# Performance work log

Measured on AMD Instinct MI355X. Metric: run time of the kernel, lower is better.

## Reference

```python
import jax, jax.numpy as jnp
import numpy as np

B, NV, L, NKG = 8, 100, 128, 923
NT = NV + 1 + NKG  # 1024 total nodes
DV, DK, DH, H, NLAYERS, VOCAB = 2048, 300, 1024, 8, 3, 50265
DHD = DH // H


def _ln(x, g, b, eps=1e-5):
    m = x.mean(-1, keepdims=True)
    v = x.var(-1, keepdims=True)
    return (x - m) / jnp.sqrt(v + eps) * g + b


def _gat_layer(x, mask, W, bb, a_src, a_dst, ln_g, ln_b):
    # x: [B,N,D], mask: [B,N,N] bool
    Bn, N, D = x.shape
    h = (x @ W + bb).reshape(Bn, N, H, DHD)
    s = jnp.einsum('bnhd,hd->bnh', h, a_src)  # source term
    t = jnp.einsum('bnhd,hd->bnh', h, a_dst)  # target term
    e = jax.nn.leaky_relu(s[:, :, None, :] + t[:, None, :, :], 0.2)  # [B,N,N,H]
    e = jnp.where(mask[..., None], e, -1e9)
    a = jax.nn.softmax(e, axis=2)  # over neighbors j
    out = jnp.einsum('bijh,bjhd->bihd', a, h).reshape(Bn, N, D)
    return _ln(x + out, ln_g, ln_b)


def setup_inputs() -> dict:
    key = jax.random.key(0)
    ks = jax.random.split(key, 24)
    s = 0.02
    inp = {
        'visual_features': jax.random.normal(ks[0], (B, NV, DV), jnp.float32),
        'question_input_ids': jax.random.randint(ks[1], (B, L), 0, VOCAB, jnp.int64) if False else jax.random.randint(ks[1], (B, L), 0, VOCAB).astype(jnp.int32),
        'question_attention_mask': jnp.ones((B, L), jnp.int32),
        'graph_node_features': jax.random.normal(ks[2], (B, NKG, DK), jnp.float32),
        'graph_adj': jax.random.randint(ks[3], (B, NT, NT), 0, 2).astype(jnp.int32),
        'graph_node_types': jax.random.randint(ks[4], (B, NT), 0, 3).astype(jnp.int32),
        # params
        'vis_W': jax.random.normal(ks[5], (DV, DH), jnp.float32) * s,
        'vis_b': jnp.zeros((DH,), jnp.float32),
        'vis_ln_g': jnp.ones((DH,), jnp.float32),
        'vis_ln_b': jnp.zeros((DH,), jnp.float32),
        'tok_emb': jax.random.normal(ks[6], (VOCAB, DH), jnp.float32) * s,
        'q_W': jax.random.normal(ks[7], (DH, DH), jnp.float32) * s,
        'q_b': jnp.zeros((DH,), jnp.float32),
        'q_ln_g': jnp.ones((DH,), jnp.float32),
        'q_ln_b': jnp.zeros((DH,), jnp.float32),
        'kg_W': jax.random.normal(ks[8], (DK, DH), jnp.float32) * s,
        'kg_b': jnp.zeros((DH,), jnp.float32),
        'kg_ln_g': jnp.ones((DH,), jnp.float32),
        'kg_ln_b': jnp.zeros((DH,), jnp.float32),
        'type_emb': jax.random.normal(ks[9], (3, DH), jnp.float32) * s,
        'gat_W': jax.random.normal(ks[10], (NLAYERS, DH, DH), jnp.float32) * s,
        'gat_b': jnp.zeros((NLAYERS, DH), jnp.float32),
        'a_src': jax.random.normal(ks[11], (NLAYERS, H, DHD), jnp.float32) * s,
        'a_dst': jax.random.normal(ks[12], (NLAYERS, H, DHD), jnp.float32) * s,
        'gat_ln_g': jnp.ones((NLAYERS, DH), jnp.float32),
        'gat_ln_b': jnp.zeros((NLAYERS, DH), jnp.float32),
        'readout_W': jax.random.normal(ks[13], (DH, 1), jnp.float32) * s,
        'readout_b': jnp.zeros((1,), jnp.float32),
        'cs_W1': jax.random.normal(ks[14], (DH, DH), jnp.float32) * s,
        'cs_b1': jnp.zeros((DH,), jnp.float32),
        'cs_W2': jax.random.normal(ks[15], (DH, 1), jnp.float32) * s,
        'cs_b2': jnp.zeros((1,), jnp.float32),
    }
    return inp


def reference(visual_features, question_input_ids, question_attention_mask,
              graph_node_features, graph_adj, graph_node_types,
              vis_W, vis_b, vis_ln_g, vis_ln_b,
              tok_emb, q_W, q_b, q_ln_g, q_ln_b,
              kg_W, kg_b, kg_ln_g, kg_ln_b,
              type_emb, gat_W, gat_b, a_src, a_dst, gat_ln_g, gat_ln_b,
              readout_W, readout_b, cs_W1, cs_b1, cs_W2, cs_b2):
    # 1. visual projection
    vis = _ln(visual_features @ vis_W + vis_b, vis_ln_g, vis_ln_b)  # [B,NV,DH]
    # 2. text encoder (embedding + masked mean-pool + proj + LN)
    te = tok_emb[question_input_ids]  # [B,L,DH]
    m = question_attention_mask.astype(te.dtype)[..., None]
    pooled = (te * m).sum(1) / jnp.maximum(m.sum(1), 1.0)
    q = _ln(pooled @ q_W + q_b, q_ln_g, q_ln_b)[:, None, :]  # [B,1,DH]
    # 3. KG projection
    kg = _ln(graph_node_features @ kg_W + kg_b, kg_ln_g, kg_ln_b)
    # 4-5. concat + node-type embeddings
    x = jnp.concatenate([vis, q, kg], axis=1) + type_emb[graph_node_types]
    # 6. dense GAT stack
    mask = graph_adj > 0
    for l in range(NLAYERS):
        x = _gat_layer(x, mask, gat_W[l], gat_b[l], a_src[l], a_dst[l],
                       gat_ln_g[l], gat_ln_b[l])
    # 7. attention-pooled readout
    w = jax.nn.softmax((x @ readout_W + readout_b).squeeze(-1), axis=-1)
    g = (x * w[..., None]).sum(1)  # [B,DH]
    # 8. candidate scorer
    logits = jax.nn.gelu(g @ cs_W1 + cs_b1) @ cs_W2 + cs_b2  # [B,1]
    return logits
```

## Files before the change

kernel.cpp:

```cpp
#include <hip/hip_runtime.h>
#include <math.h>

#define NB 8
#define NV 100
#define LQ 128
#define NKG 923
#define NT 1024
#define DV 2048
#define DK 300
#define DH 1024
#define NH 8
#define DHD 128
#define NLAYERS 3

typedef __attribute__((ext_vector_type(8))) short short8;
typedef __attribute__((ext_vector_type(4))) float f32x4;

__device__ __forceinline__ short f2bf(float f) {
    unsigned u = __float_as_uint(f);
    u += 0x7fff + ((u >> 16) & 1);
    return (short)(u >> 16);
}
__device__ __forceinline__ float bf2f(short s) {
    unsigned u = ((unsigned)(unsigned short)s) << 16;
    return __uint_as_float(u);
}
__device__ __forceinline__ unsigned pack2(float a, float b) {
    return (unsigned)(unsigned short)f2bf(a) | ((unsigned)(unsigned short)f2bf(b) << 16);
}

#if __has_builtin(__builtin_amdgcn_global_load_lds)
#define HAVE_GLL 1
__device__ __forceinline__ void gll16(const void* g, void* l) {
    __builtin_amdgcn_global_load_lds(
        (const __attribute__((address_space(1))) void*)g,
        (__attribute__((address_space(3))) void*)l, 16, 0, 0);
}
#else
#define HAVE_GLL 0
#endif

__device__ __forceinline__ float block_sum1(float a, float* red4) {
#pragma unroll
    for (int off = 32; off > 0; off >>= 1) a += __shfl_xor(a, off, 64);
    int w = threadIdx.x >> 6;
    if ((threadIdx.x & 63) == 0) red4[w] = a;
    __syncthreads();
    return red4[0] + red4[1] + red4[2] + red4[3];
}
__device__ __forceinline__ float block_max1(float a, float* red4) {
#pragma unroll
    for (int off = 32; off > 0; off >>= 1) a = fmaxf(a, __shfl_xor(a, off, 64));
    int w = threadIdx.x >> 6;
    if ((threadIdx.x & 63) == 0) red4[w] = a;
    __syncthreads();
    return fmaxf(fmaxf(red4[0], red4[1]), fmaxf(red4[2], red4[3]));
}
__device__ __forceinline__ float2 block_sum2(float a, float b, float* red8) {
#pragma unroll
    for (int off = 32; off > 0; off >>= 1) {
        a += __shfl_xor(a, off, 64);
        b += __shfl_xor(b, off, 64);
    }
    int w = threadIdx.x >> 6;
    if ((threadIdx.x & 63) == 0) { red8[w] = a; red8[4 + w] = b; }
    __syncthreads();
    float2 r;
    r.x = red8[0] + red8[1] + red8[2] + red8[3];
    r.y = red8[4] + red8[5] + red8[6] + red8[7];
    return r;
}

__global__ __launch_bounds__(256) void bitmask_kernel(
    const int* __restrict__ adj, unsigned* __restrict__ mb)
{
    int bi = blockIdx.x;
    int tid = threadIdx.x;
#pragma unroll
    for (int p = 0; p < 4; ++p) {
        int j = p * 256 + tid;
        unsigned long long bal = __ballot(adj[(size_t)bi * NT + j] > 0);
        if ((tid & 63) == 0) {
            int w = (p * 256 + (tid & 0xC0)) >> 5;
            mb[(size_t)bi * 32 + w]     = (unsigned)bal;
            mb[(size_t)bi * 32 + w + 1] = (unsigned)(bal >> 32);
        }
    }
}

__global__ __launch_bounds__(256) void transpose_cast(
    const float* __restrict__ in, short* __restrict__ out,
    int K, int N, int Kp, size_t in_stride, size_t out_stride)
{
    __shared__ float ls[64][65];
    const float* inL = in + (size_t)blockIdx.z * in_stride;
    short* outL = out + (size_t)blockIdx.z * out_stride;
    int n0 = blockIdx.x * 64, k0 = blockIdx.y * 64;
    int tid = threadIdx.x;
    int j4 = (tid & 15) * 4;
#pragma unroll
    for (int s = 0; s < 4; ++s) {
        int i = (tid >> 4) + s * 16;
        int k = k0 + i;
        float4 v = make_float4(0.f, 0.f, 0.f, 0.f);
        if (k < K) v = *(const float4*)(inL + (size_t)k * N + n0 + j4);
        ls[i][j4 + 0] = v.x; ls[i][j4 + 1] = v.y;
        ls[i][j4 + 2] = v.z; ls[i][j4 + 3] = v.w;
    }
    __syncthreads();
#pragma unroll
    for (int s = 0; s < 4; ++s) {
        int a = (tid >> 4) + s * 16;
        int b = (tid & 15) * 4;
        uint2 pk;
        pk.x = pack2(ls[b + 0][a], ls[b + 1][a]);
        pk.y = pack2(ls[b + 2][a], ls[b + 3][a]);
        *(uint2*)(outL + (size_t)(n0 + a) * Kp + k0 + b) = pk;
    }
}

__global__ __launch_bounds__(256) void gemm_bias_mfma(
    const float* __restrict__ A, const short* __restrict__ Wt,
    const float* __restrict__ bias, float* __restrict__ C,
    int M, int N, int K, int Kp, int ldA)
{
    __shared__ short At[128][32];
    __shared__ short Bt[128][32];
    int tid = threadIdx.x;
    int row0 = blockIdx.y * 128, col0 = blockIdx.x * 128;
    int lane = tid & 63, wave = tid >> 6;
    int quad = lane >> 4, lq = lane & 15;
    int wm = (wave >> 1) * 64, wn = (wave & 1) * 64;
    f32x4 acc[4][4];
#pragma unroll
    for (int i = 0; i < 4; ++i)
#pragma unroll
        for (int j = 0; j < 4; ++j) {
            f32x4 z = {0.f, 0.f, 0.f, 0.f};
            acc[i][j] = z;
        }
    int ar = tid >> 2;
    int ac = (tid & 3) * 8;
    for (int k0 = 0; k0 < Kp; k0 += 32) {
        bool fullk = (k0 + 32 <= K);
#pragma unroll
        for (int s = 0; s < 2; ++s) {
            int r = ar + s * 64;
            int grow = row0 + r;
            short8 pk;
            if (grow < M && fullk) {
                const float* src = A + (size_t)grow * ldA + k0 + ac;
                float4 v0 = *(const float4*)(src);
                float4 v1 = *(const float4*)(src + 4);
                pk[0] = f2bf(v0.x); pk[1] = f2bf(v0.y);
                pk[2] = f2bf(v0.z); pk[3] = f2bf(v0.w);
                pk[4] = f2bf(v1.x); pk[5] = f2bf(v1.y);
                pk[6] = f2bf(v1.z); pk[7] = f2bf(v1.w);
            } else {
#pragma unroll
                for (int e = 0; e < 8; ++e) {
                    int k = k0 + ac + e;
                    pk[e] = (grow < M && k < K)
                          ? f2bf(A[(size_t)grow * ldA + k]) : (short)0;
                }
            }
            *(short8*)&At[r][ac] = pk;
        }
#pragma unroll
        for (int s = 0; s < 2; ++s) {
            int n = ar + s * 64;
            short8 w = *(const short8*)(Wt + (size_t)(col0 + n) * Kp + k0 + ac);
            *(short8*)&Bt[n][ac] = w;
        }
        __syncthreads();
        short8 af[4], bfr[4];
#pragma unroll
        for (int i = 0; i < 4; ++i)
            af[i] = *(short8*)&At[wm + i * 16 + lq][quad * 8];
#pragma unroll
        for (int j = 0; j < 4; ++j)
            bfr[j] = *(short8*)&Bt[wn + j * 16 + lq][quad * 8];
#pragma unroll
        for (int i = 0; i < 4; ++i)
#pragma unroll
            for (int j = 0; j < 4; ++j)
                acc[i][j] = __builtin_amdgcn_mfma_f32_16x16x32_bf16(
                    af[i], bfr[j], acc[i][j], 0, 0, 0);
        __syncthreads();
    }
#pragma unroll
    for (int j = 0; j < 4; ++j) {
        int n = col0 + wn + j * 16 + lq;
        float bv = bias[n];
#pragma unroll
        for (int i = 0; i < 4; ++i) {
#pragma unroll
            for (int r = 0; r < 4; ++r) {
                int m = row0 + wm + i * 16 + quad * 4 + r;
                if (m < M) C[(size_t)m * N + n] = acc[i][j][r] + bv;
            }
        }
    }
}

__global__ __launch_bounds__(256) void gemm_st_mfma(
    const short* __restrict__ Ab, const short* __restrict__ Wt,
    const float* __restrict__ bias,
    const float* __restrict__ asrc, const float* __restrict__ adst,
    short* __restrict__ ht,
    float* __restrict__ sbuf, float* __restrict__ tbuf)
{
    __shared__ __align__(16) short smem[17408];
    short (*At)[32]  = (short(*)[32])smem;
    short (*Bt)[32]  = (short(*)[32])(smem + 4096);
    short (*ct)[136] = (short(*)[136])smem;
    __shared__ float sred[2][128], tred[2][128];
    __shared__ float asl[128], adl[128];
    int tid = threadIdx.x;
    int h = blockIdx.x;
    int row0 = blockIdx.y * 128, col0 = h * 128;
    int b = row0 >> 10, i0 = row0 & 1023;
    int lane = tid & 63, wave = tid >> 6;
    int quad = lane >> 4, lq = lane & 15;
    int wm = (wave >> 1) * 64, wn = (wave & 1) * 64;
    if (tid < 128) asl[tid] = asrc[h * DHD + tid];
    else adl[tid - 128] = adst[h * DHD + tid - 128];
    f32x4 acc[4][4];
#pragma unroll
    for (int i = 0; i < 4; ++i)
#pragma unroll
        for (int j = 0; j < 4; ++j) {
            f32x4 z = {0.f, 0.f, 0.f, 0.f};
            acc[i][j] = z;
        }

    const short* gA0 = Ab + (size_t)(row0 + wave * 16 + (lane >> 2)) * DH + (lane & 3) * 8;
    const short* gA1 = gA0 + (size_t)64 * DH;
    const short* gB0 = Wt + (size_t)(col0 + wave * 16 + (lane >> 2)) * DH + (lane & 3) * 8;
    const short* gB1 = gB0 + (size_t)64 * DH;
#if HAVE_GLL
    char* lA0 = (char*)At + wave * 1024; char* lA1 = lA0 + 4096;
    char* lB0 = (char*)Bt + wave * 1024; char* lB1 = lB0 + 4096;
#endif
    for (int k0 = 0; k0 < DH; k0 += 32) {
#if HAVE_GLL
        gll16(gA0 + k0, lA0); gll16(gA1 + k0, lA1);
        gll16(gB0 + k0, lB0); gll16(gB1 + k0, lB1);
#else
        {
            short8 va0 = *(const short8*)(gA0 + k0);
            short8 va1 = *(const short8*)(gA1 + k0);
            short8 vb0 = *(const short8*)(gB0 + k0);
            short8 vb1 = *(const short8*)(gB1 + k0);
            *(short8*)((char*)At + wave * 1024 + lane * 16) = va0;
            *(short8*)((char*)At + 4096 + wave * 1024 + lane * 16) = va1;
            *(short8*)((char*)Bt + wave * 1024 + lane * 16) = vb0;
            *(short8*)((char*)Bt + 4096 + wave * 1024 + lane * 16) = vb1;
        }
#endif
        __syncthreads();
        short8 af[4], bfr[4];
#pragma unroll
        for (int i = 0; i < 4; ++i)
            af[i] = *(short8*)&At[wm + i * 16 + lq][quad * 8];
#pragma unroll
        for (int j = 0; j < 4; ++j)
            bfr[j] = *(short8*)&Bt[wn + j * 16 + lq][quad * 8];
#pragma unroll
        for (int i = 0; i < 4; ++i)
#pragma unroll
            for (int j = 0; j < 4; ++j)
                acc[i][j] = __builtin_amdgcn_mfma_f32_16x16x32_bf16(
                    af[i], bfr[j], acc[i][j], 0, 0, 0);
        __syncthreads();
    }
#pragma unroll
    for (int j = 0; j < 4; ++j) {
        int d = wn + j * 16 + lq;
        float bv = bias[col0 + d];
#pragma unroll
        for (int i2 = 0; i2 < 4; ++i2) {
            int m = wm + i2 * 16 + quad * 4;
            uint2 pk;
            pk.x = pack2(acc[i2][j][0] + bv, acc[i2][j][1] + bv);
            pk.y = pack2(acc[i2][j][2] + bv, acc[i2][j][3] + bv);
            *(uint2*)&ct[d][m] = pk;
        }
    }
    __syncthreads();
    {
        int d = tid >> 1, half = tid & 1;
        short* dst = ht + ((size_t)(b * NH + h) * DHD + d) * NT + i0 + half * 64;
        const short* src = &ct[d][half * 64];
#pragma unroll
        for (int q = 0; q < 8; ++q)
            *(short8*)(dst + q * 8) = *(const short8*)(src + q * 8);
    }
    {
        int i = tid >> 1, half = tid & 1;
        float sa = 0.f, ta = 0.f;
#pragma unroll 16
        for (int dd = 0; dd < 64; ++dd) {
            int d = half * 64 + dd;
            float hv = bf2f(ct[d][i]);
            sa += hv * asl[d];
            ta += hv * adl[d];
        }
        sred[half][i] = sa; tred[half][i] = ta;
    }
    __syncthreads();
    if (tid < 128) {
        size_t idx = (size_t)(b * NH + h) * NT + i0 + tid;
        sbuf[idx] = sred[0][tid] + sred[1][tid];
        tbuf[idx] = tred[0][tid] + tred[1][tid];
    }
}

__global__ __launch_bounds__(256) void ln_scatter(
    const float* __restrict__ src, float* __restrict__ x,
    const float* __restrict__ g, const float* __restrict__ bta,
    const int* __restrict__ types, const float* __restrict__ type_emb,
    short* __restrict__ xb,
    int rows, int npb, int node_off)
{
    __shared__ float red[8];
    int r = blockIdx.x;
    if (r >= rows) return;
    int tid = threadIdx.x;
    int b = r / npb, n = r - b * npb;
    int node = b * NT + node_off + n;
    float4 v = *(const float4*)(src + (size_t)r * DH + tid * 4);
    float s = v.x + v.y + v.z + v.w;
    float sq = v.x * v.x + v.y * v.y + v.z * v.z + v.w * v.w;
    float2 t2 = block_sum2(s, sq, red);
    float mean = t2.x * (1.0f / DH);
    float var = t2.y * (1.0f / DH) - mean * mean;
    float rstd = 1.0f / sqrtf(var + 1e-5f);
    float4 gv = *(const float4*)(g + tid * 4);
    float4 bv = *(const float4*)(bta + tid * 4);
    int ty = types[node];
    float4 tv = *(const float4*)(type_emb + (size_t)ty * DH + tid * 4);
    float4 o;
    o.x = (v.x - mean) * rstd * gv.x + bv.x + tv.x;
    o.y = (v.y - mean) * rstd * gv.y + bv.y + tv.y;
    o.z = (v.z - mean) * rstd * gv.z + bv.z + tv.z;
    o.w = (v.w - mean) * rstd * gv.w + bv.w + tv.w;
    *(float4*)(x + (size_t)node * DH + tid * 4) = o;
    uint2 pk;
    pk.x = pack2(o.x, o.y);
    pk.y = pack2(o.z, o.w);
    *(uint2*)(xb + (size_t)node * DH + tid * 4) = pk;
}

__global__ __launch_bounds__(256) void ln_residual(
    float* __restrict__ x, const float* __restrict__ o,
    const float* __restrict__ g, const float* __restrict__ bta,
    short* __restrict__ xb,
    const float* __restrict__ rW, const float* __restrict__ rb,
    float* __restrict__ scores)
{
    __shared__ float red[12];
    int r = blockIdx.x;
    int tid = threadIdx.x;
    float* xr = x + (size_t)r * DH;
    float4 xv = *(float4*)(xr + tid * 4);
    float4 ov = *(const float4*)(o + (size_t)r * DH + tid * 4);
    float v0 = xv.x + ov.x, v1 = xv.y + ov.y, v2 = xv.z + ov.z, v3 = xv.w + ov.w;
    float s = v0 + v1 + v2 + v3;
    float sq = v0 * v0 + v1 * v1 + v2 * v2 + v3 * v3;
    float2 t2 = block_sum2(s, sq, red);
    float mean = t2.x * (1.0f / DH);
    float var = t2.y * (1.0f / DH) - mean * mean;
    float rstd = 1.0f / sqrtf(var + 1e-5f);
    float4 gv = *(const float4*)(g + tid * 4);
    float4 bv = *(const float4*)(bta + tid * 4);
    float4 out;
    out.x = (v0 - mean) * rstd * gv.x + bv.x;
    out.y = (v1 - mean) * rstd * gv.y + bv.y;
    out.z = (v2 - mean) * rstd * gv.z + bv.z;
    out.w = (v3 - mean) * rstd * gv.w + bv.w;
    *(float4*)(xr + tid * 4) = out;
    uint2 pk;
    pk.x = pack2(out.x, out.y);
    pk.y = pack2(out.z, out.w);
    *(uint2*)(xb + (size_t)r * DH + tid * 4) = pk;
    if (scores) {
        float4 wv = *(const float4*)(rW + tid * 4);
        float p = out.x * wv.x + out.y * wv.y + out.z * wv.z + out.w * wv.w;
        float totp = block_sum1(p, red + 8);
        if (tid == 0) scores[r] = totp + rb[0];
    }
}

__global__ __launch_bounds__(256) void qproj_fused(
    const float* __restrict__ tok_emb, const int* __restrict__ ids,
    const int* __restrict__ amask, const short* __restrict__ wt_q,
    const float* __restrict__ qb, const float* __restrict__ g,
    const float* __restrict__ bta, const int* __restrict__ types,
    const float* __restrict__ type_emb, float* __restrict__ x,
    short* __restrict__ xb)
{
    __shared__ float pl[DH];
    __shared__ float red[8];
    int b = blockIdx.x, tid = threadIdx.x;
    float a0 = 0, a1 = 0, a2 = 0, a3 = 0, denom = 0;
    for (int l = 0; l < LQ; ++l) {
        int id = ids[b * LQ + l];
        float m = (float)amask[b * LQ + l];
        denom += m;
        float4 e = *(const float4*)(tok_emb + (size_t)id * DH + tid * 4);
        a0 += m * e.x; a1 += m * e.y; a2 += m * e.z; a3 += m * e.w;
    }
    float inv = 1.0f / fmaxf(denom, 1.0f);
    pl[tid * 4 + 0] = a0 * inv; pl[tid * 4 + 1] = a1 * inv;
    pl[tid * 4 + 2] = a2 * inv; pl[tid * 4 + 3] = a3 * inv;
    __syncthreads();
    const short* w0 = wt_q + (size_t)(tid * 4 + 0) * DH;
    const short* w1 = wt_q + (size_t)(tid * 4 + 1) * DH;
    const short* w2 = wt_q + (size_t)(tid * 4 + 2) * DH;
    const short* w3 = wt_q + (size_t)(tid * 4 + 3) * DH;
    float o0 = 0, o1 = 0, o2 = 0, o3 = 0;
    for (int k0 = 0; k0 < DH; k0 += 8) {
        float4 p0 = *(const float4*)&pl[k0];
        float4 p1 = *(const float4*)&pl[k0 + 4];
        float pk[8] = {p0.x, p0.y, p0.z, p0.w, p1.x, p1.y, p1.z, p1.w};
        short8 q0 = *(const short8*)(w0 + k0);
        short8 q1 = *(const short8*)(w1 + k0);
        short8 q2 = *(const short8*)(w2 + k0);
        short8 q3 = *(const short8*)(w3 + k0);
#pragma unroll
        for (int e = 0; e < 8; ++e) {
            o0 += pk[e] * bf2f(q0[e]);
            o1 += pk[e] * bf2f(q1[e]);
            o2 += pk[e] * bf2f(q2[e]);
            o3 += pk[e] * bf2f(q3[e]);
        }
    }
    o0 += qb[tid * 4 + 0]; o1 += qb[tid * 4 + 1];
    o2 += qb[tid * 4 + 2]; o3 += qb[tid * 4 + 3];
    float s = o0 + o1 + o2 + o3;
    float sq = o0 * o0 + o1 * o1 + o2 * o2 + o3 * o3;
    float2 t2 = block_sum2(s, sq, red);
    float mean = t2.x * (1.0f / DH);
    float var = t2.y * (1.0f / DH) - mean * mean;
    float rstd = 1.0f / sqrtf(var + 1e-5f);
    float4 gv = *(const float4*)(g + tid * 4);
    float4 bv = *(const float4*)(bta + tid * 4);
    int node = b * NT + NV;
    int ty = types[node];
    float4 tv = *(const float4*)(type_emb + (size_t)ty * DH + tid * 4);
    float4 o;
    o.x = (o0 - mean) * rstd * gv.x + bv.x + tv.x;
    o.y = (o1 - mean) * rstd * gv.y + bv.y + tv.y;
    o.z = (o2 - mean) * rstd * gv.z + bv.z + tv.z;
    o.w = (o3 - mean) * rstd * gv.w + bv.w + tv.w;
    *(float4*)(x + (size_t)node * DH + tid * 4) = o;
    uint2 pk2;
    pk2.x = pack2(o.x, o.y);
    pk2.y = pack2(o.z, o.w);
    *(uint2*)(xb + (size_t)node * DH + tid * 4) = pk2;
}

__global__ __launch_bounds__(256) void agg_mfma(
    const short* __restrict__ ht, const unsigned* __restrict__ mb,
    const float* __restrict__ s, const float* __restrict__ t,
    float* __restrict__ obuf)
{
    __shared__ __align__(16) short vt[2][128 * 64];
    __shared__ short at[64][72];
    __shared__ unsigned mrow[64][32];
    __shared__ float sv[64], alpha_s[64], lfin[64];
    int i0 = blockIdx.x * 64;
    int h = blockIdx.y, b = blockIdx.z;
    int tid = threadIdx.x;
    int lane = tid & 63, wave = tid >> 6;
    int quad = lane >> 4, lq = lane & 15;
    int wi = (wave >> 1) * 32;
    int wd = (wave & 1) * 64;
    if (tid < 64) sv[tid] = s[(size_t)(b * NH + h) * NT + i0 + tid];
#pragma unroll
    for (int s2 = 0; s2 < 2; ++s2) {
        int f = tid + s2 * 256;
        int ii2 = f >> 3, w4 = (f & 7) * 4;
        *(uint4*)&mrow[ii2][w4] =
            *(const uint4*)(mb + ((size_t)(b * NT + i0 + ii2)) * 32 + w4);
    }
    const float* tptr = t + (size_t)(b * NH + h) * NT;
    const short* hbase = ht + ((size_t)(b * NH + h) * DHD) * NT;
    const short* gsrc[4];
#pragma unroll
    for (int s2 = 0; s2 < 4; ++s2) {
        int f = tid + s2 * 256;
        int d = f >> 3, cc = f & 7;
        gsrc[s2] = hbase + (size_t)d * NT + ((cc ^ (d & 7)) * 8);
    }
    f32x4 acc[2][4];
#pragma unroll
    for (int i = 0; i < 2; ++i)
#pragma unroll
        for (int j = 0; j < 4; ++j) {
            f32x4 z = {0.f, 0.f, 0.f, 0.f};
            acc[i][j] = z;
        }
    int ii = tid >> 2;
    int jq = (tid & 3) * 16;
    float m_run = -3e38f, l_run = 0.f;
    __syncthreads();
    {
        char* d0 = (char*)(&vt[0][0]) + wave * 1024;
#if HAVE_GLL
#pragma unroll
        for (int s2 = 0; s2 < 4; ++s2) gll16(gsrc[s2], d0 + s2 * 4096);
#else
#pragma unroll
        for (int s2 = 0; s2 < 4; ++s2) {
            int f = tid + s2 * 256;
            short8 v8 = *(const short8*)(gsrc[s2]);
            *(short8*)((char*)(&vt[0][0]) + (size_t)f * 16) = v8;
        }
#endif
    }
    for (int it = 0; it < 16; ++it) {
        int j0 = it * 64;
        int cur = it & 1;
        int jn = (j0 + 64 < NT) ? j0 + 64 : j0;
        float4 t0 = *(const float4*)(tptr + j0 + jq);
        float4 t1 = *(const float4*)(tptr + j0 + jq + 4);
        float4 t2 = *(const float4*)(tptr + j0 + jq + 8);
        float4 t3 = *(const float4*)(tptr + j0 + jq + 12);
        {
            char* dn = (char*)(&vt[cur ^ 1][0]) + wave * 1024;
#if HAVE_GLL
#pragma unroll
            for (int s2 = 0; s2 < 4; ++s2) gll16(gsrc[s2] + jn, dn + s2 * 4096);
#else
#pragma unroll
            for (int s2 = 0; s2 < 4; ++s2) {
                int f = tid + s2 * 256;
                short8 v8 = *(const short8*)(gsrc[s2] + jn);
                *(short8*)((char*)(&vt[cur ^ 1][0]) + (size_t)f * 16) = v8;
            }
#endif
        }
        float vv[16];
        unsigned mw;
        float tmax = -3e38f;
        {
            mw = mrow[ii][(j0 + jq) >> 5] >> ((j0 + jq) & 31);
            float svv = sv[ii];
            float tv16[16] = {t0.x, t0.y, t0.z, t0.w, t1.x, t1.y, t1.z, t1.w,
                              t2.x, t2.y, t2.z, t2.w, t3.x, t3.y, t3.z, t3.w};
#pragma unroll
            for (int e = 0; e < 16; ++e) {
                float v = svv + tv16[e];
                v = v > 0.f ? v : 0.2f * v;
                v = ((mw >> e) & 1) ? v : -1e9f;
                vv[e] = v;
                tmax = fmaxf(tmax, v);
            }
        }
        tmax = fmaxf(tmax, __shfl_xor(tmax, 1, 64));
        tmax = fmaxf(tmax, __shfl_xor(tmax, 2, 64));
        float m_new = fmaxf(m_run, tmax);
        float al = __expf(m_run - m_new);
        float tsum = 0.f;
        short8 p0, p1;
#pragma unroll
        for (int e = 0; e < 8; ++e) {
            float w = ((mw >> e) & 1) ? __expf(vv[e] - m_new) : 0.f;
            tsum += w; p0[e] = f2bf(w);
        }
#pragma unroll
        for (int e = 0; e < 8; ++e) {
            float w = ((mw >> (8 + e)) & 1) ? __expf(vv[8 + e] - m_new) : 0.f;
            tsum += w; p1[e] = f2bf(w);
        }
        tsum += __shfl_xor(tsum, 1, 64);
        tsum += __shfl_xor(tsum, 2, 64);
        l_run = l_run * al + tsum;
        m_run = m_new;
        *(short8*)&at[ii][jq] = p0;
        *(short8*)&at[ii][jq + 8] = p1;
        if ((tid & 3) == 0) alpha_s[ii] = al;
        asm volatile("s_waitcnt lgkmcnt(0)" ::: "memory");
        __builtin_amdgcn_s_barrier();
#pragma unroll
        for (int i2 = 0; i2 < 2; ++i2)
#pragma unroll
            for (int r = 0; r < 4; ++r) {
                float arow = alpha_s[wi + i2 * 16 + quad * 4 + r];
#pragma unroll
                for (int j = 0; j < 4; ++j) acc[i2][j][r] *= arow;
            }
        const char* vtb = (const char*)(&vt[cur][0]);
#pragma unroll
        for (int ks = 0; ks < 2; ++ks) {
            short8 af[2], bfr[4];
            af[0] = *(short8*)&at[wi + lq][ks * 32 + quad * 8];
            af[1] = *(short8*)&at[wi + 16 + lq][ks * 32 + quad * 8];
            int cc = ks * 4 + quad;
            int sx = (cc ^ (lq & 7)) * 16;
#pragma unroll
            for (int j = 0; j < 4; ++j)
                bfr[j] = *(const short8*)(vtb + (wd + j * 16 + lq) * 128 + sx);
#pragma unroll
            for (int i2 = 0; i2 < 2; ++i2)
#pragma unroll
                for (int j = 0; j < 4; ++j)
                    acc[i2][j] = __builtin_amdgcn_mfma_f32_16x16x32_bf16(
                        af[i2], bfr[j], acc[i2][j], 0, 0, 0);
        }
        __builtin_amdgcn_s_barrier();
    }
    if ((tid & 3) == 0) lfin[ii] = l_run;
    __syncthreads();
#pragma unroll
    for (int i2 = 0; i2 < 2; ++i2) {
#pragma unroll
        for (int r = 0; r < 4; ++r) {
            int il = wi + i2 * 16 + quad * 4 + r;
            float inv = 1.0f / lfin[il];
            float* dst = obuf + ((size_t)(b * NT + i0 + il)) * DH + h * DHD + wd;
#pragma unroll
            for (int j = 0; j < 4; ++j)
                dst[j * 16 + lq] = acc[i2][j][r] * inv;
        }
    }
}

__global__ __launch_bounds__(256) void pool_part(
    const float* __restrict__ x, const float* __restrict__ scores,
    float* __restrict__ gpart)
{
    __shared__ float red[8];
    int p = blockIdx.x;
    int b = blockIdx.y;
    int tid = threadIdx.x;
    const float* sr = scores + (size_t)b * NT;
    float v[4];
    float mx = -3e38f;
#pragma unroll
    for (int k = 0; k < 4; ++k) { v[k] = sr[tid + k * 256]; mx = fmaxf(mx, v[k]); }
    float m = block_max1(mx, red);
    float ls = 0.f;
#pragma unroll
    for (int k = 0; k < 4; ++k) ls += expf(v[k] - m);
    float tot = block_sum1(ls, red + 4);
    float inv = 1.0f / tot;
    float a0 = 0, a1 = 0, a2 = 0, a3 = 0;
    for (int n = p * 128; n < (p + 1) * 128; ++n) {
        float wv = expf(sr[n] - m) * inv;
        float4 xv = *(const float4*)(x + ((size_t)(b * NT + n)) * DH + tid * 4);
        a0 += wv * xv.x; a1 += wv * xv.y; a2 += wv * xv.z; a3 += wv * xv.w;
    }
    float4 o = make_float4(a0, a1, a2, a3);
    *(float4*)(gpart + ((size_t)(b * 8 + p)) * DH + tid * 4) = o;
}

__global__ __launch_bounds__(256) void scorer_part(
    const float* __restrict__ gpart, const float* __restrict__ W1,
    float* __restrict__ spart)
{
    __shared__ float gsh[128];
    int c = blockIdx.x, b = blockIdx.y;
    int tid = threadIdx.x;
    if (tid < 128) {
        int d = c * 128 + tid;
        float gv = 0.f;
#pragma unroll
        for (int p = 0; p < 8; ++p) gv += gpart[((size_t)(b * 8 + p)) * DH + d];
        gsh[tid] = gv;
    }
    __syncthreads();
    float acc[4] = {};
    for (int dd = 0; dd < 128; ++dd) {
        float gv = gsh[dd];
        const float* wr = W1 + (size_t)(c * 128 + dd) * DH;
#pragma unroll
        for (int cc = 0; cc < 4; ++cc) acc[cc] += gv * wr[tid + cc * 256];
    }
#pragma unroll
    for (int cc = 0; cc < 4; ++cc)
        spart[((size_t)(b * 8 + c)) * DH + tid + cc * 256] = acc[cc];
}
__global__ __launch_bounds__(256) void scorer_fin(
    const float* __restrict__ spart, const float* __restrict__ b1,
    const float* __restrict__ W2, const float* __restrict__ b2,
    float* __restrict__ out)
{
    __shared__ float red[4];
    int b = blockIdx.x;
    int tid = threadIdx.x;
    float part = 0.f;
#pragma unroll
    for (int cc = 0; cc < 4; ++cc) {
        int k = tid + cc * 256;
        float s = 0.f;
#pragma unroll
        for (int c = 0; c < 8; ++c) s += spart[((size_t)(b * 8 + c)) * DH + k];
        float u = s + b1[k];
        float inner = 0.7978845608028654f * (u + 0.044715f * u * u * u);
        float gel = 0.5f * u * (1.0f + tanhf(inner));
        part += gel * W2[k];
    }
    float tot = block_sum1(part, red);
    if (tid == 0) out[b] = tot + b2[0];
}

extern "C" void kernel_launch(void* const* d_in, const int* in_sizes, int n_in,
                              void* d_out, int out_size, void* d_ws, size_t ws_size,
                              hipStream_t stream)
{
    const float* visual   = (const float*)d_in[0];
    const int*   q_ids    = (const int*)d_in[1];
    const int*   q_mask   = (const int*)d_in[2];
    const float* kg_feat  = (const float*)d_in[3];
    const int*   adj      = (const int*)d_in[4];
    const int*   ntypes   = (const int*)d_in[5];
    const float* vis_W    = (const float*)d_in[6];
    const float* vis_b    = (const float*)d_in[7];
    const float* vis_lng  = (const float*)d_in[8];
    const float* vis_lnb  = (const float*)d_in[9];
    const float* tok_emb  = (const float*)d_in[10];
    const float* q_W      = (const float*)d_in[11];
    const float* q_b      = (const float*)d_in[12];
    const float* q_lng    = (const float*)d_in[13];
    const float* q_lnb    = (const float*)d_in[14];
    const float* kg_W     = (const float*)d_in[15];
    const float* kg_b     = (const float*)d_in[16];
    const float* kg_lng   = (const float*)d_in[17];
    const float* kg_lnb   = (const float*)d_in[18];
    const float* type_emb = (const float*)d_in[19];
    const float* gat_W    = (const float*)d_in[20];
    const float* gat_b    = (const float*)d_in[21];
    const float* a_src    = (const float*)d_in[22];
    const float* a_dst    = (const float*)d_in[23];
    const float* gat_lng  = (const float*)d_in[24];
    const float* gat_lnb  = (const float*)d_in[25];
    const float* read_W   = (const float*)d_in[26];
    const float* read_b   = (const float*)d_in[27];
    const float* cs_W1    = (const float*)d_in[28];
    const float* cs_b1    = (const float*)d_in[29];
    const float* cs_W2    = (const float*)d_in[30];
    const float* cs_b2    = (const float*)d_in[31];
    float* out = (float*)d_out;

    float* ws = (float*)d_ws;
    const size_t NROW = (size_t)NB * NT;
    float* x      = ws;
    float* obuf   = x + NROW * DH;
    float* sbuf   = obuf + NROW * DH;
    float* tbuf   = sbuf + NB * NH * NT;
    float* pooled = tbuf + NB * NH * NT;
    float* scores = pooled + NB * DH;
    float* gpart  = scores + NROW;
    float* ppool  = gpart + NB * 8 * DH;
    float* pden   = ppool + NB * 4 * DH;
    float* spart  = pden + 64;
    short* wt_gat = (short*)(spart + NB * 8 * DH);
    short* ht     = wt_gat + (size_t)NLAYERS * DH * DH;
    unsigned* mb  = (unsigned*)(ht + (size_t)NB * NH * DHD * NT);
    short* xb     = (short*)(mb + (size_t)NB * NT * 32);
    short* wt_vis = xb + NROW * DH;
    short* wt_q   = wt_vis + (size_t)1024 * 2048;
    short* wt_kg  = wt_q + (size_t)1024 * 1024;

    transpose_cast<<<dim3(16, 32, 1), 256, 0, stream>>>(vis_W, wt_vis, DV, DH, DV, 0, 0);
    transpose_cast<<<dim3(16, 16, 1), 256, 0, stream>>>(q_W, wt_q, DH, DH, DH, 0, 0);
    transpose_cast<<<dim3(16, 5, 1), 256, 0, stream>>>(kg_W, wt_kg, DK, DH, 320, 0, 0);
    transpose_cast<<<dim3(16, 16, NLAYERS), 256, 0, stream>>>(
        gat_W, wt_gat, DH, DH, DH, (size_t)DH * DH, (size_t)DH * DH);
    bitmask_kernel<<<NB * NT, 256, 0, stream>>>(adj, mb);

    gemm_bias_mfma<<<dim3(8, 7), 256, 0, stream>>>(
        visual, wt_vis, vis_b, obuf, NB * NV, DH, DV, DV, DV);
    ln_scatter<<<NB * NV, 256, 0, stream>>>(obuf, x, vis_lng, vis_lnb,
        ntypes, type_emb, xb, NB * NV, NV, 0);

    qproj_fused<<<NB, 256, 0, stream>>>(tok_emb, q_ids, q_mask, wt_q,
        q_b, q_lng, q_lnb, ntypes, type_emb, x, xb);

    gemm_bias_mfma<<<dim3(8, 58), 256, 0, stream>>>(
        kg_feat, wt_kg, kg_b, obuf, NB * NKG, DH, DK, 320, DK);
    ln_scatter<<<NB * NKG, 256, 0, stream>>>(obuf, x, kg_lng, kg_lnb,
        ntypes, type_emb, xb, NB * NKG, NKG, NV + 1);

    for (int l = 0; l < NLAYERS; ++l) {
        const float* bl  = gat_b + (size_t)l * DH;
        const float* asl = a_src + (size_t)l * NH * DHD;
        const float* adl = a_dst + (size_t)l * NH * DHD;
        gemm_st_mfma<<<dim3(NH, 64), 256, 0, stream>>>(
            xb, wt_gat + (size_t)l * DH * DH, bl, asl, adl, ht, sbuf, tbuf);
        agg_mfma<<<dim3(16, NH, NB), 256, 0, stream>>>(
            ht, mb, sbuf, tbuf, obuf);
        ln_residual<<<NB * NT, 256, 0, stream>>>(x, obuf,
            gat_lng + (size_t)l * DH, gat_lnb + (size_t)l * DH, xb,
            read_W, read_b, (l == NLAYERS - 1) ? scores : nullptr);
    }

    pool_part<<<dim3(8, NB), 256, 0, stream>>>(x, scores, gpart);
    scorer_part<<<dim3(8, NB), 256, 0, stream>>>(gpart, cs_W1, spart);
    scorer_fin<<<NB, 256, 0, stream>>>(spart, cs_b1, cs_W2, cs_b2, out);
}
```

Measured before the change: 981.4 us.

## Single-buffer GAT aggregation tiles and split token pooling across waves

The aggregation kernel drops its double-buffered V tile and the prefetch of the next tile. It now loads each 64-column tile into one LDS buffer behind a full __syncthreads at the top of every iteration. This halves the V-tile LDS footprint, which may allow more resident blocks, but it stops overlapping global loads with the softmax/MFMA work. Separately, the question pooling kernel splits the 128 tokens across four waves, each accumulating full rows, and reduces the partial sums through shared memory, giving more independent loads per thread.

```diff
diff --git a/kernel.cpp b/kernel.cpp
--- a/kernel.cpp
+++ b/kernel.cpp
@@ -400,20 +400,46 @@
     const float* __restrict__ type_emb, float* __restrict__ x,
     short* __restrict__ xb)
 {
+    __shared__ float pws[4][DH];
     __shared__ float pl[DH];
+    __shared__ float pden4[4];
     __shared__ float red[8];
     int b = blockIdx.x, tid = threadIdx.x;
-    float a0 = 0, a1 = 0, a2 = 0, a3 = 0, denom = 0;
-    for (int l = 0; l < LQ; ++l) {
+    int wv = tid >> 6, lane = tid & 63;
+    float pa[4][4] = {};
+    float denom = 0.f;
+    for (int i = 0; i < 32; ++i) {
+        int l = wv * 32 + i;
         int id = ids[b * LQ + l];
         float m = (float)amask[b * LQ + l];
         denom += m;
-        float4 e = *(const float4*)(tok_emb + (size_t)id * DH + tid * 4);
-        a0 += m * e.x; a1 += m * e.y; a2 += m * e.z; a3 += m * e.w;
-    }
-    float inv = 1.0f / fmaxf(denom, 1.0f);
-    pl[tid * 4 + 0] = a0 * inv; pl[tid * 4 + 1] = a1 * inv;
-    pl[tid * 4 + 2] = a2 * inv; pl[tid * 4 + 3] = a3 * inv;
+        const float* er = tok_emb + (size_t)id * DH + lane * 4;
+#pragma unroll
+        for (int gg = 0; gg < 4; ++gg) {
+            float4 e = *(const float4*)(er + gg * 256);
+            pa[gg][0] += m * e.x; pa[gg][1] += m * e.y;
+            pa[gg][2] += m * e.z; pa[gg][3] += m * e.w;
+        }
+    }
+#pragma unroll
+    for (int gg = 0; gg < 4; ++gg)
+        *(float4*)&pws[wv][gg * 256 + lane * 4] =
+            make_float4(pa[gg][0], pa[gg][1], pa[gg][2], pa[gg][3]);
+    if (lane == 0) pden4[wv] = denom;
+    __syncthreads();
+    {
+        float dtot = pden4[0] + pden4[1] + pden4[2] + pden4[3];
+        float inv = 1.0f / fmaxf(dtot, 1.0f);
+        int d0 = tid * 4;
+        float4 s0 = *(const float4*)&pws[0][d0];
+        float4 s1 = *(const float4*)&pws[1][d0];
+        float4 s2 = *(const float4*)&pws[2][d0];
+        float4 s3 = *(const float4*)&pws[3][d0];
+        pl[d0 + 0] = (s0.x + s1.x + s2.x + s3.x) * inv;
+        pl[d0 + 1] = (s0.y + s1.y + s2.y + s3.y) * inv;
+        pl[d0 + 2] = (s0.z + s1.z + s2.z + s3.z) * inv;
+        pl[d0 + 3] = (s0.w + s1.w + s2.w + s3.w) * inv;
+    }
     __syncthreads();
     const short* w0 = wt_q + (size_t)(tid * 4 + 0) * DH;
     const short* w1 = wt_q + (size_t)(tid * 4 + 1) * DH;
@@ -466,7 +492,7 @@
     const float* __restrict__ s, const float* __restrict__ t,
     float* __restrict__ obuf)
 {
-    __shared__ __align__(16) short vt[2][128 * 64];
+    __shared__ __align__(16) short vt[128 * 64];
     __shared__ short at[64][72];
     __shared__ unsigned mrow[64][32];
     __shared__ float sv[64], alpha_s[64], lfin[64];
@@ -488,11 +514,13 @@
     const float* tptr = t + (size_t)(b * NH + h) * NT;
     const short* hbase = ht + ((size_t)(b * NH + h) * DHD) * NT;
     const short* gsrc[4];
+    char* ldst[4];
 #pragma unroll
     for (int s2 = 0; s2 < 4; ++s2) {
         int f = tid + s2 * 256;
         int d = f >> 3, cc = f & 7;
         gsrc[s2] = hbase + (size_t)d * NT + ((cc ^ (d & 7)) * 8);
+        ldst[s2] = (char*)vt + wave * 1024 + s2 * 4096;
     }
     f32x4 acc[2][4];
 #pragma unroll
@@ -505,49 +533,29 @@
     int ii = tid >> 2;
     int jq = (tid & 3) * 16;
     float m_run = -3e38f, l_run = 0.f;
-    __syncthreads();
-    {
-        char* d0 = (char*)(&vt[0][0]) + wave * 1024;
+    for (int j0 = 0; j0 < NT; j0 += 64) {
+        __syncthreads();
 #if HAVE_GLL
 #pragma unroll
-        for (int s2 = 0; s2 < 4; ++s2) gll16(gsrc[s2], d0 + s2 * 4096);
+        for (int s2 = 0; s2 < 4; ++s2) gll16(gsrc[s2] + j0, ldst[s2]);
 #else
 #pragma unroll
         for (int s2 = 0; s2 < 4; ++s2) {
             int f = tid + s2 * 256;
-            short8 v8 = *(const short8*)(gsrc[s2]);
-            *(short8*)((char*)(&vt[0][0]) + (size_t)f * 16) = v8;
+            short8 v8 = *(const short8*)(gsrc[s2] + j0);
+            *(short8*)((char*)vt + (size_t)f * 16) = v8;
         }
 #endif
-    }
-    for (int it = 0; it < 16; ++it) {
-        int j0 = it * 64;
-        int cur = it & 1;
-        int jn = (j0 + 64 < NT) ? j0 + 64 : j0;
-        float4 t0 = *(const float4*)(tptr + j0 + jq);
-        float4 t1 = *(const float4*)(tptr + j0 + jq + 4);
-        float4 t2 = *(const float4*)(tptr + j0 + jq + 8);
-        float4 t3 = *(const float4*)(tptr + j0 + jq + 12);
-        {
-            char* dn = (char*)(&vt[cur ^ 1][0]) + wave * 1024;
-#if HAVE_GLL
-#pragma unroll
-            for (int s2 = 0; s2 < 4; ++s2) gll16(gsrc[s2] + jn, dn + s2 * 4096);
-#else
-#pragma unroll
-            for (int s2 = 0; s2 < 4; ++s2) {
-                int f = tid + s2 * 256;
-                short8 v8 = *(const short8*)(gsrc[s2] + jn);
-                *(short8*)((char*)(&vt[cur ^ 1][0]) + (size_t)f * 16) = v8;
-            }
-#endif
-        }
         float vv[16];
         unsigned mw;
         float tmax = -3e38f;
         {
             mw = mrow[ii][(j0 + jq) >> 5] >> ((j0 + jq) & 31);
             float svv = sv[ii];
+            float4 t0 = *(const float4*)(tptr + j0 + jq);
+            float4 t1 = *(const float4*)(tptr + j0 + jq + 4);
+            float4 t2 = *(const float4*)(tptr + j0 + jq + 8);
+            float4 t3 = *(const float4*)(tptr + j0 + jq + 12);
             float tv16[16] = {t0.x, t0.y, t0.z, t0.w, t1.x, t1.y, t1.z, t1.w,
                               t2.x, t2.y, t2.z, t2.w, t3.x, t3.y, t3.z, t3.w};
 #pragma unroll
@@ -582,8 +590,7 @@
         *(short8*)&at[ii][jq] = p0;
         *(short8*)&at[ii][jq + 8] = p1;
         if ((tid & 3) == 0) alpha_s[ii] = al;
-        asm volatile("s_waitcnt lgkmcnt(0)" ::: "memory");
-        __builtin_amdgcn_s_barrier();
+        __syncthreads();
 #pragma unroll
         for (int i2 = 0; i2 < 2; ++i2)
 #pragma unroll
@@ -592,7 +599,7 @@
 #pragma unroll
                 for (int j = 0; j < 4; ++j) acc[i2][j][r] *= arow;
             }
-        const char* vtb = (const char*)(&vt[cur][0]);
+        const char* vtb = (const char*)vt;
 #pragma unroll
         for (int ks = 0; ks < 2; ++ks) {
             short8 af[2], bfr[4];
@@ -610,7 +617,6 @@
                     acc[i2][j] = __builtin_amdgcn_mfma_f32_16x16x32_bf16(
                         af[i2], bfr[j], acc[i2][j], 0, 0, 0);
         }
-        __builtin_amdgcn_s_barrier();
     }
     if ((tid & 3) == 0) lfin[ii] = l_run;
     __syncthreads();
```

Measured after the change: 959.5 us. -2.2%, faster.
